# Optimization experiments

Measured on AMD Instinct MI355X. Metric: run time of the kernel, lower is better.

The kernel has to match this reference:

```python
import jax, jax.numpy as jnp
import numpy as np

NUM_EMBEDDINGS = 8192
EMBEDDING_DIM = 256
COMMITMENT_COST = 0.25
DECAY = 0.99
EPS = 1e-05


def setup_inputs() -> dict:
    key = jax.random.key(0)
    k1, k2, k3 = jax.random.split(key, 3)
    x = jax.random.normal(k1, (16, 256, 32, 32), dtype=jnp.float32)
    emb = jax.random.normal(k2, (NUM_EMBEDDINGS, EMBEDDING_DIM), dtype=jnp.float32) * 0.1
    emb = emb / jnp.linalg.norm(emb, axis=1, keepdims=True)  # F.normalize(dim=1)
    return {
        "x": x,
        "embedding": emb,
        "cluster_size": jnp.ones((NUM_EMBEDDINGS,), dtype=jnp.float32),
        "embed_avg": emb,
    }


def reference(x, embedding, cluster_size, embed_avg):
    K, D = embedding.shape
    n = x.ndim
    # permute channels (dim 1) to last, flatten to [N, D]
    perm_fwd = (0,) + tuple(range(2, n)) + (1,)
    px = jnp.transpose(x, perm_fwd)
    flat = px.reshape(-1, D)  # [N, D]

    # squared L2 distances (monotone in cdist p=2) -> argmin nearest code
    d = (
        jnp.sum(flat * flat, axis=1, keepdims=True)
        - 2.0 * (flat @ embedding.T)
        + jnp.sum(embedding * embedding, axis=1)
    )  # [N, K]
    idx = jnp.argmin(d, axis=1)  # [N]

    # gather-by-index instead of one-hot @ embedding (same math)
    quantized = embedding[idx].reshape(px.shape)
    perm_back = (0, n - 1) + tuple(range(1, n - 1))
    quantized = jnp.transpose(quantized, perm_back)  # back to x layout

    # EMA buffer updates (training path, no_grad in torch)
    counts = jax.ops.segment_sum(
        jnp.ones_like(idx, dtype=flat.dtype), idx, num_segments=K
    )  # == encodings.sum(0)
    new_cluster_size = cluster_size * DECAY + (1.0 - DECAY) * counts
    dw = jax.ops.segment_sum(flat, idx, num_segments=K)  # == encodings.T @ flat
    new_embed_avg = embed_avg * DECAY + (1.0 - DECAY) * dw
    new_embedding = new_embed_avg / jnp.maximum(new_cluster_size, EPS)[:, None]

    # commitment loss (quantized detached)
    loss = COMMITMENT_COST * jnp.mean((x - jax.lax.stop_gradient(quantized)) ** 2)

    # straight-through estimator
    quantized_st = x + jax.lax.stop_gradient(quantized - x)

    avg_probs = counts / flat.shape[0]  # == encodings.mean(0)
    perplexity = jnp.exp(-jnp.sum(avg_probs * jnp.log(avg_probs + 1e-10)))

    return (quantized_st, loss, perplexity, new_embedding, new_cluster_size, new_embed_avg)
```

## Files before the change

kernel.cpp:

```cpp
#include <hip/hip_runtime.h>
#include <stdint.h>

#define K_CODES 8192
#define D 256
#define NROWS 16384
#define NELEM 4194304

#define WS_ENORM   0x00000u
#define WS_KEYS    0x08000u
#define WS_ICOUNTS 0x28000u
#define WS_CURSOR  0x30000u
#define WS_BASE    0x38000u
#define WS_ROWLIST 0x40000u
#define WS_PART    0x50000u
#define WS_XHI     0x60000u
#define WS_XLO     (WS_XHI + 0x800000u)
#define WS_EHI     (WS_XLO + 0x800000u)
#define WS_ELO     (WS_EHI + 0x400000u)

#define O_QST  0
#define O_LOSS 4194304
#define O_PERP 4194305
#define O_EMB  4194306
#define O_CS   6291458
#define O_EAVG 6299650

typedef unsigned short u16;
typedef __attribute__((ext_vector_type(8))) short bf16x8;
typedef __attribute__((ext_vector_type(4))) float f32x4;

__device__ __forceinline__ u16 f2bf(float f) {
    uint32_t u = __float_as_uint(f);
    u += 0x7FFFu + ((u >> 16) & 1u);
    return (u16)(u >> 16);
}
__device__ __forceinline__ float bf2f(u16 h) {
    return __uint_as_float(((uint32_t)h) << 16);
}

__device__ __forceinline__ void glds16(const u16* g, u16* lds_base) {
    __builtin_amdgcn_global_load_lds(
        (const __attribute__((address_space(1))) uint32_t*)g,
        (__attribute__((address_space(3))) uint32_t*)lds_base, 16, 0, 0);
}

__global__ __launch_bounds__(256) void prep_emb_kernel(const float* __restrict__ emb,
                                                       u16* __restrict__ eh,
                                                       u16* __restrict__ el,
                                                       float* __restrict__ enorm) {
    const int k = blockIdx.x, t = threadIdx.x;
    const size_t i = (size_t)k * D + t;
    const float v = emb[i];
    const u16 h = f2bf(v);
    const float r = v - bf2f(h);
    eh[i] = h;
    el[i] = f2bf(r);
    float s = v * v;
#pragma unroll
    for (int off = 32; off; off >>= 1) s += __shfl_down(s, off, 64);
    __shared__ float sm[4];
    if ((t & 63) == 0) sm[t >> 6] = s;
    __syncthreads();
    if (t == 0) enorm[k] = sm[0] + sm[1] + sm[2] + sm[3];
}

__global__ __launch_bounds__(256) void prep_x_kernel(const float* __restrict__ x,
                                                     u16* __restrict__ xhi,
                                                     u16* __restrict__ xlo) {
    __shared__ u16 Lh[64][72];
    __shared__ u16 Ll[64][72];
    const int hw0 = blockIdx.x << 6;
    const int c0 = blockIdx.y << 6;
    const int b = blockIdx.z;
    const int t = threadIdx.x, l = t & 63, w = t >> 6;
#pragma unroll
    for (int i = 0; i < 16; ++i) {
        const int cl = w * 16 + i;
        const float v = x[(((size_t)(b * 256 + c0 + cl)) << 10) + hw0 + l];
        const u16 h = f2bf(v);
        Lh[l][cl] = h;
        Ll[l][cl] = f2bf(v - bf2f(h));
    }
    __syncthreads();
    const int r = t >> 2, cs = t & 3;
    const size_t n = (((size_t)b) << 10) + hw0 + r;
    const size_t o = n * D + c0 + cs * 16;
    *(uint4*)&xhi[o]     = *(const uint4*)&Lh[r][cs * 16];
    *(uint4*)&xhi[o + 8] = *(const uint4*)&Lh[r][cs * 16 + 8];
    *(uint4*)&xlo[o]     = *(const uint4*)&Ll[r][cs * 16];
    *(uint4*)&xlo[o + 8] = *(const uint4*)&Ll[r][cs * 16 + 8];
}

#define BM 128
#define BN 128
#define SLICES 2
#define CT_PER 32

__global__ __launch_bounds__(256, 1) void dist_kernel(const u16* __restrict__ xhi,
                                                      const u16* __restrict__ xlo,
                                                      const u16* __restrict__ ehi,
                                                      const u16* __restrict__ elo,
                                                      const float* __restrict__ enorm,
                                                      unsigned long long* __restrict__ keys) {
    extern __shared__ __align__(16) u16 lds[];

    const int tid = threadIdx.x;
    const int l = tid & 63, w = tid >> 6;
    const int wr = w >> 1, wc = w & 1;
    const int slice = blockIdx.x;
    const int n0 = blockIdx.y * BM;
    const int md = l & 15, quad = l >> 4;

#pragma unroll
    for (int wd = 0; wd < 16; ++wd) {
        const int win = w * 16 + wd;
        const int rA = 2 * win + (l >> 5);
        const int g = (l & 31) ^ (rA & 31);
        const size_t src = (size_t)(n0 + rA) * D + g * 8;
        glds16(xhi + src, &lds[win * 512]);
        glds16(xlo + src, &lds[32768 + win * 512]);
    }

    const int rloc = l >> 3, sB = l & 7, gB = sB ^ rloc;
    const u16* PB[4];
#pragma unroll
    for (int w8 = 0; w8 < 4; ++w8) {
        const u16* pl = (gB & 4) ? elo : ehi;
        PB[w8] = pl + (size_t)(slice * 4096 + w * 32 + w8 * 8 + rloc) * D + (gB & 3) * 8;
    }
    const int bdst = 65536 + (w * 32) * 64;

#pragma unroll
    for (int w8 = 0; w8 < 4; ++w8) glds16(PB[w8], &lds[bdst + w8 * 512]);

    int rbase[4], rh[4];
#pragma unroll
    for (int i = 0; i < 4; ++i) {
        const int rA = wr * 64 + i * 16 + md;
        rbase[i] = rA * 256;
        rh[i] = rA & 31;
    }
    int offBH[4], offBL[4];
#pragma unroll
    for (int j = 0; j < 4; ++j) {
        const int cr = wc * 64 + j * 16 + md;
        offBH[j] = 65536 + cr * 64 + ((quad) ^ (md & 7)) * 8;
        offBL[j] = 65536 + cr * 64 + ((quad + 4) ^ (md & 7)) * 8;
    }

    float rbv[4][4];
    int rbi[4][4];
#pragma unroll
    for (int i = 0; i < 4; ++i)
#pragma unroll
        for (int r = 0; r < 4; ++r) { rbv[i][r] = 1e30f; rbi[i][r] = 0; }

    for (int ct = 0; ct < CT_PER; ++ct) {
        f32x4 acc[4][4];
#pragma unroll
        for (int i = 0; i < 4; ++i)
#pragma unroll
            for (int j = 0; j < 4; ++j) acc[i][j] = (f32x4)0.f;

#pragma unroll
        for (int kt = 0; kt < 8; ++kt) {
            __syncthreads();
            const int m = ct * 8 + kt;
            if (m < CT_PER * 8 - 1) {
                const int m1 = m + 1;
                const int soff = (m1 >> 3) * 32768 + (m1 & 7) * 32;
                const int db = bdst + ((m1 & 1) << 13);
#pragma unroll
                for (int w8 = 0; w8 < 4; ++w8)
                    glds16(PB[w8] + soff, &lds[db + w8 * 512]);
            }

            const int bufo = (kt & 1) << 13;
            bf16x8 ah[4], al4[4], bh4[4], bl4[4];
#pragma unroll
            for (int i = 0; i < 4; ++i) {
                const int slot = ((kt << 2) | quad) ^ rh[i];
                ah[i]  = *(const bf16x8*)&lds[rbase[i] + slot * 8];
                al4[i] = *(const bf16x8*)&lds[32768 + rbase[i] + slot * 8];
            }
#pragma unroll
            for (int j = 0; j < 4; ++j) {
                bh4[j] = *(const bf16x8*)&lds[bufo + offBH[j]];
                bl4[j] = *(const bf16x8*)&lds[bufo + offBL[j]];
            }
#pragma unroll
            for (int i = 0; i < 4; ++i)
#pragma unroll
                for (int j = 0; j < 4; ++j) {
                    acc[i][j] = __builtin_amdgcn_mfma_f32_16x16x32_bf16(ah[i],  bh4[j], acc[i][j], 0, 0, 0);
                    acc[i][j] = __builtin_amdgcn_mfma_f32_16x16x32_bf16(ah[i],  bl4[j], acc[i][j], 0, 0, 0);
                    acc[i][j] = __builtin_amdgcn_mfma_f32_16x16x32_bf16(al4[i], bh4[j], acc[i][j], 0, 0, 0);
                }
        }

        const int gc0 = slice * 4096 + ct * 128;
        float ec[4];
#pragma unroll
        for (int j = 0; j < 4; ++j) ec[j] = enorm[gc0 + wc * 64 + j * 16 + md];
#pragma unroll
        for (int i = 0; i < 4; ++i)
#pragma unroll
            for (int r = 0; r < 4; ++r)
#pragma unroll
                for (int j = 0; j < 4; ++j) {
                    const float s = fmaf(-2.f, acc[i][j][r], ec[j]);
                    const int ci = gc0 + wc * 64 + j * 16 + md;
                    if (s < rbv[i][r]) { rbv[i][r] = s; rbi[i][r] = ci; }
                }
    }

#pragma unroll
    for (int i = 0; i < 4; ++i)
#pragma unroll
        for (int r = 0; r < 4; ++r) {
            float bv = rbv[i][r];
            int bi = rbi[i][r];
#pragma unroll
            for (int m = 1; m < 16; m <<= 1) {
                const float ov = __shfl_xor(bv, m, 64);
                const int oi = __shfl_xor(bi, m, 64);
                if (ov < bv || (ov == bv && oi < bi)) { bv = ov; bi = oi; }
            }
            if (md == 0) {
                unsigned int u = __float_as_uint(bv);
                u = (u & 0x80000000u) ? ~u : (u | 0x80000000u);
                const unsigned long long key = ((unsigned long long)u << 32) | (unsigned int)bi;
                atomicMin(&keys[n0 + wr * 64 + i * 16 + quad * 4 + r], key);
            }
        }
}

__global__ __launch_bounds__(256) void quant_loss_kernel(const float* __restrict__ x,
                                                         const float* __restrict__ emb,
                                                         const unsigned long long* __restrict__ keys,
                                                         float* __restrict__ out,
                                                         float* __restrict__ partials,
                                                         int* __restrict__ icounts) {
    const int blk = blockIdx.x;
    const int b = blk >> 4;
    const int hw0 = (blk & 15) << 6;
    const int l = threadIdx.x & 63;
    const int cq = threadIdx.x >> 6;
    const int hw = hw0 + l;
    const int n = (b << 10) + hw;
    const int code = (int)(keys[n] & 0xFFFFFFFFull);
    if (threadIdx.x < 64) atomicAdd(&icounts[code], 1);
    const float* erow = emb + (size_t)code * D;
    const float* xb = x + (((size_t)b * 256) << 10) + hw;
    float* ob = out + O_QST + (((size_t)b * 256) << 10) + hw;
    float lsum = 0.f;
#pragma unroll 4
    for (int c = cq; c < D; c += 4) {
        const float xv = xb[(size_t)c << 10];
        const float ev = erow[c];
        ob[(size_t)c << 10] = xv + (ev - xv);
        const float d = xv - ev;
        lsum = fmaf(d, d, lsum);
    }
    __shared__ float sm[4];
    const int lane = threadIdx.x & 63, wv = threadIdx.x >> 6;
#pragma unroll
    for (int off = 32; off; off >>= 1) lsum += __shfl_down(lsum, off, 64);
    if (lane == 0) sm[wv] = lsum;
    __syncthreads();
    if (threadIdx.x == 0) partials[blockIdx.x] = sm[0] + sm[1] + sm[2] + sm[3];
}

__global__ __launch_bounds__(256) void scan_final_kernel(const int* __restrict__ icounts,
                                                         int* __restrict__ basearr,
                                                         const float* __restrict__ partials,
                                                         float* __restrict__ out) {
    const int t = threadIdx.x, lane = t & 63, w = t >> 6;
    int loc = 0;
    float ps = 0.f;
    for (int i = 0; i < 32; ++i) {
        const int c = icounts[t * 32 + i];
        loc += c;
        const float p = (float)c * (1.0f / 16384.0f);
        ps += p * logf(p + 1e-10f);
    }
    int v = loc;
#pragma unroll
    for (int off = 1; off < 64; off <<= 1) {
        const int u = __shfl_up(v, off, 64);
        if (lane >= off) v += u;
    }
    __shared__ int wsum[4];
    __shared__ float fs[8];
    if (lane == 63) wsum[w] = v;
    float lp = partials[t];
#pragma unroll
    for (int off = 32; off; off >>= 1) {
        lp += __shfl_down(lp, off, 64);
        ps += __shfl_down(ps, off, 64);
    }
    if (lane == 0) { fs[w] = lp; fs[4 + w] = ps; }
    __syncthreads();
    int pre = 0;
    for (int i = 0; i < w; ++i) pre += wsum[i];
    int b = pre + v - loc;
    for (int i = 0; i < 32; ++i) {
        basearr[t * 32 + i] = b;
        b += icounts[t * 32 + i];
    }
    if (t == 0) {
        out[O_LOSS] = 0.25f * ((fs[0] + fs[1] + fs[2] + fs[3]) / 4194304.0f);
        out[O_PERP] = expf(-(fs[4] + fs[5] + fs[6] + fs[7]));
    }
}

__global__ __launch_bounds__(256) void slot_kernel(const unsigned long long* __restrict__ keys,
                                                   const int* __restrict__ basearr,
                                                   int* __restrict__ cursor,
                                                   int* __restrict__ rowlist) {
    const int n = blockIdx.x * 256 + threadIdx.x;
    const int code = (int)(keys[n] & 0xFFFFFFFFull);
    const int pos = atomicAdd(&cursor[code], 1);
    rowlist[basearr[code] + pos] = n;
}

__global__ __launch_bounds__(256) void gather_ema_kernel(const u16* __restrict__ xhi,
                                                         const u16* __restrict__ xlo,
                                                         const int* __restrict__ icounts,
                                                         const int* __restrict__ basearr,
                                                         const int* __restrict__ rowlist,
                                                         const float* __restrict__ embed_avg,
                                                         const float* __restrict__ cluster_size,
                                                         float* __restrict__ out) {
    const int k = blockIdx.x, c = threadIdx.x;
    const int cnt = icounts[k], b0 = basearr[k];
    float s = 0.f;
    for (int t = 0; t < cnt; ++t) {
        const int n = rowlist[b0 + t];
        s += bf2f(xhi[(size_t)n * D + c]) + bf2f(xlo[(size_t)n * D + c]);
    }
    const float ncs = cluster_size[k] * 0.99f + 0.01f * (float)cnt;
    const size_t i = (size_t)k * D + c;
    const float na = embed_avg[i] * 0.99f + 0.01f * s;
    out[O_EAVG + i] = na;
    out[O_EMB + i] = na / fmaxf(ncs, 1e-5f);
    if (c == 0) out[O_CS + k] = ncs;
}

extern "C" void kernel_launch(void* const* d_in, const int* in_sizes, int n_in,
                              void* d_out, int out_size, void* d_ws, size_t ws_size,
                              hipStream_t stream) {
    const float* x            = (const float*)d_in[0];
    const float* emb          = (const float*)d_in[1];
    const float* cluster_size = (const float*)d_in[2];
    const float* embed_avg    = (const float*)d_in[3];
    float* out = (float*)d_out;
    char* ws = (char*)d_ws;

    float* enorm = (float*)(ws + WS_ENORM);
    unsigned long long* keys = (unsigned long long*)(ws + WS_KEYS);
    int* icounts = (int*)(ws + WS_ICOUNTS);
    int* cursor = (int*)(ws + WS_CURSOR);
    int* basearr = (int*)(ws + WS_BASE);
    int* rowlist = (int*)(ws + WS_ROWLIST);
    float* partials = (float*)(ws + WS_PART);
    u16* xhi = (u16*)(ws + WS_XHI);
    u16* xlo = (u16*)(ws + WS_XLO);
    u16* ehi = (u16*)(ws + WS_EHI);
    u16* elo = (u16*)(ws + WS_ELO);

    static int lds_attr_set = 0;
    if (!lds_attr_set) {
        hipFuncSetAttribute((const void*)dist_kernel,
                            hipFuncAttributeMaxDynamicSharedMemorySize, 163840);
        lds_attr_set = 1;
    }

    hipMemsetAsync(ws + WS_ICOUNTS, 0, 0x10000, stream);
    hipMemsetAsync(ws + WS_KEYS, 0xFF, NROWS * 8, stream);

    prep_emb_kernel<<<K_CODES, 256, 0, stream>>>(emb, ehi, elo, enorm);
    prep_x_kernel<<<dim3(16, 4, 16), 256, 0, stream>>>(x, xhi, xlo);
    dist_kernel<<<dim3(SLICES, NROWS / BM), 256, 163840, stream>>>(xhi, xlo, ehi, elo, enorm, keys);
    quant_loss_kernel<<<256, 256, 0, stream>>>(x, emb, keys, out, partials, icounts);
    scan_final_kernel<<<1, 256, 0, stream>>>(icounts, basearr, partials, out);
    slot_kernel<<<NROWS / 256, 256, 0, stream>>>(keys, basearr, cursor, rowlist);
    gather_ema_kernel<<<K_CODES, 256, 0, stream>>>(xhi, xlo, icounts, basearr, rowlist,
                                                   embed_avg, cluster_size, out);
}
```

Before: 298.7 us.

## Software-pipeline LDS fragment loads against MFMAs with register double buffering

Keeps two sets of A/B bf16 fragments in registers so LDS reads for the next k-step are issued before the MFMAs for the previous step, hiding LDS latency. The accumulator reset and distance/argmin epilogue for each code tile are moved into the first k-step of the following tile, with a drain step after the loop. The code-norm loads are prefetched one tile ahead. The doubled fragment registers raise VGPR pressure and may lower occupancy or cause spills.

```diff
diff --git a/kernel.cpp b/kernel.cpp
--- a/kernel.cpp
+++ b/kernel.cpp
@@ -155,60 +155,95 @@
 #pragma unroll
         for (int r = 0; r < 4; ++r) { rbv[i][r] = 1e30f; rbi[i][r] = 0; }
 
+    f32x4 acc[4][4];
+#pragma unroll
+    for (int i = 0; i < 4; ++i)
+#pragma unroll
+        for (int j = 0; j < 4; ++j) acc[i][j] = (f32x4)0.f;
+
+    bf16x8 fah[2][4], fal[2][4], fbh[2][4], fbl[2][4];
+
+    float ecr[4];
+#pragma unroll
+    for (int j = 0; j < 4; ++j) ecr[j] = enorm[slice * 4096 + wc * 64 + j * 16 + md];
+
     for (int ct = 0; ct < CT_PER; ++ct) {
-        f32x4 acc[4][4];
-#pragma unroll
-        for (int i = 0; i < 4; ++i)
-#pragma unroll
-            for (int j = 0; j < 4; ++j) acc[i][j] = (f32x4)0.f;
-
 #pragma unroll
         for (int kt = 0; kt < 8; ++kt) {
             __syncthreads();
-            const int m = ct * 8 + kt;
-            if (m < CT_PER * 8 - 1) {
-                const int m1 = m + 1;
-                const int soff = (m1 >> 3) * 32768 + (m1 & 7) * 32;
-                const int db = bdst + ((m1 & 1) << 13);
-#pragma unroll
-                for (int w8 = 0; w8 < 4; ++w8)
-                    glds16(PB[w8] + soff, &lds[db + w8 * 512]);
-            }
-
-            const int bufo = (kt & 1) << 13;
-            bf16x8 ah[4], al4[4], bh4[4], bl4[4];
+            if (kt < 7) {
+                const int soff = ct * 32768 + (kt + 1) * 32;
+                const int db = bdst + (((kt + 1) & 1) << 13);
+#pragma unroll
+                for (int w8 = 0; w8 < 4; ++w8) glds16(PB[w8] + soff, &lds[db + w8 * 512]);
+            } else if (ct < CT_PER - 1) {
+                const int soff = (ct + 1) * 32768;
+#pragma unroll
+                for (int w8 = 0; w8 < 4; ++w8) glds16(PB[w8] + soff, &lds[bdst + w8 * 512]);
+            }
+            const int p = kt & 1, bufo = p << 13;
 #pragma unroll
             for (int i = 0; i < 4; ++i) {
                 const int slot = ((kt << 2) | quad) ^ rh[i];
-                ah[i]  = *(const bf16x8*)&lds[rbase[i] + slot * 8];
-                al4[i] = *(const bf16x8*)&lds[32768 + rbase[i] + slot * 8];
+                fah[p][i] = *(const bf16x8*)&lds[rbase[i] + slot * 8];
+                fal[p][i] = *(const bf16x8*)&lds[32768 + rbase[i] + slot * 8];
             }
 #pragma unroll
             for (int j = 0; j < 4; ++j) {
-                bh4[j] = *(const bf16x8*)&lds[bufo + offBH[j]];
-                bl4[j] = *(const bf16x8*)&lds[bufo + offBL[j]];
-            }
-#pragma unroll
-            for (int i = 0; i < 4; ++i)
+                fbh[p][j] = *(const bf16x8*)&lds[bufo + offBH[j]];
+                fbl[p][j] = *(const bf16x8*)&lds[bufo + offBL[j]];
+            }
+            if (kt > 0 || ct > 0) {
+                const int q = p ^ 1;
+#pragma unroll
+                for (int i = 0; i < 4; ++i)
+#pragma unroll
+                    for (int j = 0; j < 4; ++j) {
+                        acc[i][j] = __builtin_amdgcn_mfma_f32_16x16x32_bf16(fah[q][i], fbh[q][j], acc[i][j], 0, 0, 0);
+                        acc[i][j] = __builtin_amdgcn_mfma_f32_16x16x32_bf16(fah[q][i], fbl[q][j], acc[i][j], 0, 0, 0);
+                        acc[i][j] = __builtin_amdgcn_mfma_f32_16x16x32_bf16(fal[q][i], fbh[q][j], acc[i][j], 0, 0, 0);
+                    }
+                if (kt == 0) {
+                    const int gc0 = slice * 4096 + (ct - 1) * 128;
+#pragma unroll
+                    for (int i = 0; i < 4; ++i)
+#pragma unroll
+                        for (int r = 0; r < 4; ++r)
+#pragma unroll
+                            for (int j = 0; j < 4; ++j) {
+                                const float s = fmaf(-2.f, acc[i][j][r], ecr[j]);
+                                const int ci = gc0 + wc * 64 + j * 16 + md;
+                                if (s < rbv[i][r]) { rbv[i][r] = s; rbi[i][r] = ci; }
+                            }
+#pragma unroll
+                    for (int j = 0; j < 4; ++j)
+                        ecr[j] = enorm[slice * 4096 + ct * 128 + wc * 64 + j * 16 + md];
+#pragma unroll
+                    for (int i = 0; i < 4; ++i)
+#pragma unroll
+                        for (int j = 0; j < 4; ++j) acc[i][j] = (f32x4)0.f;
+                }
+            }
+        }
+    }
+
+    {
+#pragma unroll
+        for (int i = 0; i < 4; ++i)
+#pragma unroll
+            for (int j = 0; j < 4; ++j) {
+                acc[i][j] = __builtin_amdgcn_mfma_f32_16x16x32_bf16(fah[1][i], fbh[1][j], acc[i][j], 0, 0, 0);
+                acc[i][j] = __builtin_amdgcn_mfma_f32_16x16x32_bf16(fah[1][i], fbl[1][j], acc[i][j], 0, 0, 0);
+                acc[i][j] = __builtin_amdgcn_mfma_f32_16x16x32_bf16(fal[1][i], fbh[1][j], acc[i][j], 0, 0, 0);
+            }
+        const int gc0 = slice * 4096 + (CT_PER - 1) * 128;
+#pragma unroll
+        for (int i = 0; i < 4; ++i)
+#pragma unroll
+            for (int r = 0; r < 4; ++r)
 #pragma unroll
                 for (int j = 0; j < 4; ++j) {
-                    acc[i][j] = __builtin_amdgcn_mfma_f32_16x16x32_bf16(ah[i],  bh4[j], acc[i][j], 0, 0, 0);
-                    acc[i][j] = __builtin_amdgcn_mfma_f32_16x16x32_bf16(ah[i],  bl4[j], acc[i][j], 0, 0, 0);
-                    acc[i][j] = __builtin_amdgcn_mfma_f32_16x16x32_bf16(al4[i], bh4[j], acc[i][j], 0, 0, 0);
-                }
-        }
-
-        const int gc0 = slice * 4096 + ct * 128;
-        float ec[4];
-#pragma unroll
-        for (int j = 0; j < 4; ++j) ec[j] = enorm[gc0 + wc * 64 + j * 16 + md];
-#pragma unroll
-        for (int i = 0; i < 4; ++i)
-#pragma unroll
-            for (int r = 0; r < 4; ++r)
-#pragma unroll
-                for (int j = 0; j < 4; ++j) {
-                    const float s = fmaf(-2.f, acc[i][j][r], ec[j]);
+                    const float s = fmaf(-2.f, acc[i][j][r], ecr[j]);
                     const int ci = gc0 + wc * 64 + j * 16 + md;
                     if (s < rbv[i][r]) { rbv[i][r] = s; rbi[i][r] = ci; }
                 }
```

After: 301.6 us. About the same (+1.0%).
